# Performance work log

Hardware: AMD Instinct MI355X
Metric: run time of the kernel (lower is better)

The kernel has to match this reference:

```python
import jax, jax.numpy as jnp
import numpy as np

B, T, D, H = 16, 4096, 256, 512  # batch, seq_len, ninputs, nhiddens


def setup_inputs() -> dict:
    key = jax.random.key(0)
    k_x, k_ih, k_hh, k_b, k_bn = jax.random.split(key, 5)
    s = 1.0 / np.sqrt(H)
    xs = jax.random.normal(k_x, (B, T, D), dtype=jnp.float32)
    W_ih = jax.random.uniform(k_ih, (3 * H, D), minval=-s, maxval=s, dtype=jnp.float32)
    W_hh = jax.random.uniform(k_hh, (3 * H, H), minval=-s, maxval=s, dtype=jnp.float32)
    b = jax.random.uniform(k_b, (3 * H,), minval=-s, maxval=s, dtype=jnp.float32)
    b_n = jax.random.uniform(k_bn, (H,), minval=-s, maxval=s, dtype=jnp.float32)
    return {"xs": xs, "W_ih": W_ih, "W_hh": W_hh, "b": b, "b_n": b_n}


def _gru_scan(xs, W_ih, W_hh, b, b_n):
    # Precompute all input-side gates with one big GEMM: (B, T, 3H)
    igates = jnp.einsum('btd,gd->btg', xs, W_ih) + b

    def step(h, ig):
        # h: (B, H), ig: (B, 3H)
        hg = h @ W_hh.T  # (B, 3H)
        i_r, i_z, i_n = jnp.split(ig, 3, axis=-1)
        h_r, h_z, h_n = jnp.split(hg, 3, axis=-1)
        r = jax.nn.sigmoid(i_r + h_r)   # reset gate
        z = jax.nn.sigmoid(i_z + h_z)   # update gate (equinox 'inp')
        n = jnp.tanh(i_n + r * (h_n + b_n))
        h_new = n + z * (h - n)         # equinox: new + inp * (hidden - new)
        return h_new, h_new

    h0 = jnp.zeros((xs.shape[0], b_n.shape[0]), dtype=xs.dtype)
    _, ys = jax.lax.scan(step, h0, jnp.swapaxes(igates, 0, 1))  # (T, B, H)
    return jnp.swapaxes(ys, 0, 1)  # (B, T, H)


def reference(xs, W_ih, W_hh, b, b_n):
    # CellLayer('gru', 'deer') computes the exact GRU recurrence over time
    # (DEER's fixed point equals the sequential evaluation).
    return _gru_scan(xs, W_ih, W_hh, b, b_n)
```

## Files before the change

kernel.cpp:

```cpp
#include <hip/hip_runtime.h>
#include <stdint.h>
#include <stddef.h>

#define B_ 16
#define T_ 4096
#define D_ 256
#define H_ 512
#define G3_ 1536

#define OFF_IG   ((size_t)0)
#define OFF_WT   ((size_t)201326592)
#define OFF_MB   ((size_t)202899456)
#define WS_NEED  ((size_t)203423744)

#define PAR_STRIDE ((size_t)B_ * 8 * 512)

typedef _Float16 h2_t __attribute__((ext_vector_type(2)));

#if defined(__has_builtin)
#if __has_builtin(__builtin_amdgcn_fdot2)
#define HAVE_FDOT2 1
#endif
#endif

__device__ __forceinline__ float fdot2f(uint32_t w, uint32_t h, float acc) {
  union { uint32_t u; h2_t v; } a, b;
  a.u = w; b.u = h;
#ifdef HAVE_FDOT2
  return __builtin_amdgcn_fdot2(a.v, b.v, acc, false);
#else
  return fmaf((float)a.v.x, (float)b.v.x, fmaf((float)a.v.y, (float)b.v.y, acc));
#endif
}

__device__ __forceinline__ uint32_t packh2(float a, float b) {
  union { h2_t v; uint32_t u; } x;
  x.v.x = (_Float16)a; x.v.y = (_Float16)b;
  return x.u;
}

__device__ __forceinline__ uint32_t f16bits(float a) {
  union { _Float16 h; uint16_t u; } x;
  x.h = (_Float16)a;
  return (uint32_t)x.u;
}

__device__ __forceinline__ float h2f(uint16_t u) {
  union { _Float16 h; uint16_t u; } x;
  x.u = u;
  return (float)x.h;
}

__device__ __forceinline__ float sigmoidf_(float x) {
  return 1.0f / (1.0f + __expf(-x));
}

__device__ __forceinline__ float tanhf_(float x) {
  x = fminf(fmaxf(x, -15.0f), 15.0f);
  float e = __expf(-2.0f * x);
  return (1.0f - e) / (1.0f + e);
}

__global__ void __launch_bounds__(256) wt_kernel(const float* __restrict__ W, float4* __restrict__ Wt4) {
  int idx = blockIdx.x * 256 + threadIdx.x;
  if (idx >= G3_ * 64) return;
  int g = idx % G3_;
  int d4 = idx / G3_;
  float4 v = *(const float4*)(W + (size_t)g * D_ + 4 * d4);
  Wt4[(size_t)d4 * G3_ + g] = v;
}

__global__ void __launch_bounds__(256) ig_kernel(const float* __restrict__ xs,
                                                 const float* __restrict__ Wt,
                                                 const float* __restrict__ bias,
                                                 _Float16* __restrict__ ig) {
  __shared__ float xls[16 * 256];
  const int m0 = blockIdx.x * 16;
  const int tid = threadIdx.x;

  const float4* xsrc = (const float4*)(xs + (size_t)m0 * D_);
  float4* xdst = (float4*)xls;
#pragma unroll
  for (int k = 0; k < 4; ++k) xdst[tid + 256 * k] = xsrc[tid + 256 * k];
  __syncthreads();

  float acc[6][16];
#pragma unroll
  for (int k = 0; k < 6; ++k)
#pragma unroll
    for (int m = 0; m < 16; ++m) acc[k][m] = 0.0f;

  const float4* Wt4 = (const float4*)Wt;
  const float4* lds4 = (const float4*)xls;

  for (int d4 = 0; d4 < 64; ++d4) {
    float4 w[6];
#pragma unroll
    for (int k = 0; k < 6; ++k) w[k] = Wt4[(size_t)d4 * G3_ + tid + 256 * k];
#pragma unroll
    for (int m = 0; m < 16; ++m) {
      float4 xv = lds4[m * 64 + d4];
#pragma unroll
      for (int k = 0; k < 6; ++k) {
        acc[k][m] = fmaf(w[k].x, xv.x, acc[k][m]);
        acc[k][m] = fmaf(w[k].y, xv.y, acc[k][m]);
        acc[k][m] = fmaf(w[k].z, xv.z, acc[k][m]);
        acc[k][m] = fmaf(w[k].w, xv.w, acc[k][m]);
      }
    }
  }

#pragma unroll
  for (int k = 0; k < 6; ++k) {
    float bb = bias[tid + 256 * k];
#pragma unroll
    for (int m = 0; m < 16; ++m) {
      ig[(size_t)(m0 + m) * G3_ + tid + 256 * k] = (_Float16)(acc[k][m] + bb);
    }
  }
}

__global__ void __launch_bounds__(256, 1) rec_kernel(const _Float16* __restrict__ ig,
                                                     const float* __restrict__ Whh,
                                                     const float* __restrict__ bn,
                                                     uint32_t* __restrict__ mb,
                                                     float* __restrict__ out) {
  const int tid = threadIdx.x;
  const int wg = blockIdx.x;
  const int b = wg >> 4;
  const int s = wg & 15;
  const int q = tid & 7;
  const int c = tid >> 3;
  const int j = s * 32 + c;

  uint32_t wr[32], wz[32], wn[32];
  {
    const float4* s0 = (const float4*)(Whh + (size_t)j * H_ + q * 64);
    const float4* s1 = (const float4*)(Whh + (size_t)(j + H_) * H_ + q * 64);
    const float4* s2 = (const float4*)(Whh + (size_t)(j + 2 * H_) * H_ + q * 64);
#pragma unroll
    for (int i = 0; i < 16; ++i) {
      float4 v0 = s0[i]; wr[2 * i] = packh2(v0.x, v0.y); wr[2 * i + 1] = packh2(v0.z, v0.w);
      float4 v1 = s1[i]; wz[2 * i] = packh2(v1.x, v1.y); wz[2 * i + 1] = packh2(v1.z, v1.w);
      float4 v2 = s2[i]; wn[2 * i] = packh2(v2.x, v2.y); wn[2 * i + 1] = packh2(v2.z, v2.w);
    }
  }
  const float bnj = bn[j];

  __shared__ uint32_t hl[2][8][36];

  uint32_t* mypoll = mb + ((size_t)b * 8 + (s >> 1)) * 512 + 2 * tid;
  uint32_t* mypub  = mb + ((size_t)b * 8 + q) * 512 + j;

  const uint16_t* ig16 = (const uint16_t*)ig;
  size_t igbase = (size_t)b * T_ * G3_;

  uint16_t cr = ig16[igbase + j];
  uint16_t cz = ig16[igbase + j + H_];
  uint16_t cn = ig16[igbase + j + 2 * H_];
  uint16_t nr = ig16[igbase + G3_ + j];
  uint16_t nz = ig16[igbase + G3_ + j + H_];
  uint16_t nn2 = ig16[igbase + G3_ + j + 2 * H_];

  float hprev = 0.0f;

  for (int t = 0; t < T_; ++t) {
    uint16_t fr = 0, fz = 0, fn = 0;

    if (t > 0) {
      uint32_t* pb = mypoll + (size_t)(t & 1) * PAR_STRIDE;
      const uint32_t hi = (uint32_t)t << 16;
      uint32_t a0, a1;
      int it = 0;
      for (;;) {
        unsigned long long vv;
        asm volatile("global_load_dwordx2 %0, %1, off sc1\n\ts_waitcnt vmcnt(0)"
                     : "=v"(vv) : "v"(pb) : "memory");
        a0 = (uint32_t)vv;
        a1 = (uint32_t)(vv >> 32);
        if ((((a0 ^ hi) | (a1 ^ hi)) >> 16) == 0u) break;
        if (++it > (1 << 20)) { a0 = a1 = 0x7C00u; break; }
      }
      hl[t & 1][tid >> 5][tid & 31] = (a0 & 0xFFFFu) | (a1 << 16);

      if (t + 2 < T_) {
        const size_t fb = igbase + 2 * (size_t)G3_;
        fr = ig16[fb + j];
        fz = ig16[fb + j + H_];
        fn = ig16[fb + j + 2 * H_];
      }
    } else {
      const size_t fb = igbase + 2 * (size_t)G3_;
      fr = ig16[fb + j];
      fz = ig16[fb + j + H_];
      fn = ig16[fb + j + 2 * H_];
    }

    __syncthreads();

    float ar = 0.0f, az = 0.0f, an = 0.0f;
    if (t > 0) {
      const uint4* hq = (const uint4*)hl[t & 1][q];
      uint4 hv[8];
#pragma unroll
      for (int i = 0; i < 8; ++i) hv[i] = hq[i];
      float ar0 = 0.0f, az0 = 0.0f, an0 = 0.0f;
      float ar1 = 0.0f, az1 = 0.0f, an1 = 0.0f;
#pragma unroll
      for (int i = 0; i < 4; ++i) {
        ar0 = fdot2f(wr[4 * i + 0], hv[i].x, ar0); az0 = fdot2f(wz[4 * i + 0], hv[i].x, az0); an0 = fdot2f(wn[4 * i + 0], hv[i].x, an0);
        ar0 = fdot2f(wr[4 * i + 1], hv[i].y, ar0); az0 = fdot2f(wz[4 * i + 1], hv[i].y, az0); an0 = fdot2f(wn[4 * i + 1], hv[i].y, an0);
        ar0 = fdot2f(wr[4 * i + 2], hv[i].z, ar0); az0 = fdot2f(wz[4 * i + 2], hv[i].z, az0); an0 = fdot2f(wn[4 * i + 2], hv[i].z, an0);
        ar0 = fdot2f(wr[4 * i + 3], hv[i].w, ar0); az0 = fdot2f(wz[4 * i + 3], hv[i].w, az0); an0 = fdot2f(wn[4 * i + 3], hv[i].w, an0);
      }
#pragma unroll
      for (int i = 4; i < 8; ++i) {
        ar1 = fdot2f(wr[4 * i + 0], hv[i].x, ar1); az1 = fdot2f(wz[4 * i + 0], hv[i].x, az1); an1 = fdot2f(wn[4 * i + 0], hv[i].x, an1);
        ar1 = fdot2f(wr[4 * i + 1], hv[i].y, ar1); az1 = fdot2f(wz[4 * i + 1], hv[i].y, az1); an1 = fdot2f(wn[4 * i + 1], hv[i].y, an1);
        ar1 = fdot2f(wr[4 * i + 2], hv[i].z, ar1); az1 = fdot2f(wz[4 * i + 2], hv[i].z, az1); an1 = fdot2f(wn[4 * i + 2], hv[i].z, an1);
        ar1 = fdot2f(wr[4 * i + 3], hv[i].w, ar1); az1 = fdot2f(wz[4 * i + 3], hv[i].w, az1); an1 = fdot2f(wn[4 * i + 3], hv[i].w, an1);
      }
      ar = ar0 + ar1; az = az0 + az1; an = an0 + an1;
      ar += __shfl_xor(ar, 1); ar += __shfl_xor(ar, 2); ar += __shfl_xor(ar, 4);
      az += __shfl_xor(az, 1); az += __shfl_xor(az, 2); az += __shfl_xor(az, 4);
      an += __shfl_xor(an, 1); an += __shfl_xor(an, 2); an += __shfl_xor(an, 4);
    }

    const float igr = h2f(cr), igz = h2f(cz), ign = h2f(cn);
    const float r = sigmoidf_(igr + ar);
    const float z = sigmoidf_(igz + az);
    const float n = tanhf_(ign + r * (an + bnj));
    const float hnew = n + z * (hprev - n);
    hprev = hnew;

    const uint32_t wv = ((uint32_t)(t + 1) << 16) | f16bits(hnew);
    __hip_atomic_store(mypub + (size_t)((t + 1) & 1) * PAR_STRIDE, wv,
                       __ATOMIC_RELAXED, __HIP_MEMORY_SCOPE_AGENT);

    if (q == 0) {
      out[((size_t)b * T_ + t) * H_ + j] = hnew;
    }

    cr = nr; cz = nz; cn = nn2;
    nr = fr; nz = fz; nn2 = fn;
    igbase += G3_;
  }
}

__global__ void __launch_bounds__(512) naive_kernel(const float* __restrict__ xs,
                                                    const float* __restrict__ Wih,
                                                    const float* __restrict__ Whh,
                                                    const float* __restrict__ bias,
                                                    const float* __restrict__ bn,
                                                    float* __restrict__ out) {
  const int b = blockIdx.x;
  const int j = threadIdx.x;
  __shared__ float h[H_];
  __shared__ float xr[D_];
  h[j] = 0.0f;
  __syncthreads();
  for (int t = 0; t < T_; ++t) {
    if (j < D_) xr[j] = xs[((size_t)b * T_ + t) * D_ + j];
    __syncthreads();
    float a[2];
#pragma unroll
    for (int g = 0; g < 2; ++g) {
      const int row = j + g * H_;
      float ssum = bias[row];
      const float* wi = Wih + (size_t)row * D_;
      for (int d = 0; d < D_; ++d) ssum = fmaf(wi[d], xr[d], ssum);
      const float* wh = Whh + (size_t)row * H_;
      for (int kk = 0; kk < H_; ++kk) ssum = fmaf(wh[kk], h[kk], ssum);
      a[g] = ssum;
    }
    const float r = sigmoidf_(a[0]);
    const float z = sigmoidf_(a[1]);
    float i_n = bias[j + 2 * H_];
    {
      const float* wi = Wih + (size_t)(j + 2 * H_) * D_;
      for (int d = 0; d < D_; ++d) i_n = fmaf(wi[d], xr[d], i_n);
    }
    float h_n = 0.0f;
    {
      const float* wh = Whh + (size_t)(j + 2 * H_) * H_;
      for (int kk = 0; kk < H_; ++kk) h_n = fmaf(wh[kk], h[kk], h_n);
    }
    const float nn = tanhf_(i_n + r * (h_n + bn[j]));
    const float hnew = nn + z * (h[j] - nn);
    __syncthreads();
    h[j] = hnew;
    out[((size_t)b * T_ + t) * H_ + j] = hnew;
  }
}

extern "C" void kernel_launch(void* const* d_in, const int* in_sizes, int n_in,
                              void* d_out, int out_size, void* d_ws, size_t ws_size,
                              hipStream_t stream) {
  const float* xs  = (const float*)d_in[0];
  const float* Wih = (const float*)d_in[1];
  const float* Whh = (const float*)d_in[2];
  const float* bia = (const float*)d_in[3];
  const float* bnp = (const float*)d_in[4];
  float* out = (float*)d_out;

  if (ws_size >= WS_NEED) {
    char* ws = (char*)d_ws;
    _Float16* igp = (_Float16*)(ws + OFF_IG);
    float* wtp = (float*)(ws + OFF_WT);
    uint32_t* mbp = (uint32_t*)(ws + OFF_MB);

    hipMemsetAsync(mbp, 0, 2 * PAR_STRIDE * sizeof(uint32_t), stream);

    wt_kernel<<<dim3(384), dim3(256), 0, stream>>>(Wih, (float4*)wtp);
    ig_kernel<<<dim3((B_ * T_) / 16), dim3(256), 0, stream>>>(xs, wtp, bia, igp);
    rec_kernel<<<dim3(256), dim3(256), 0, stream>>>(igp, Whh, bnp, mbp, out);
  } else {
    naive_kernel<<<dim3(B_), dim3(H_), 0, stream>>>(xs, Wih, Whh, bia, bnp, out);
  }
}
```

Baseline: 7.599 ms.

## Remap workgroups so each batch shares an XCD and poll a local mailbox first

Workgroup indices are remapped so the 16 workgroups of one batch land on the same XCD, given round-robin dispatch across the 8 XCDs. Each step's hidden state is now published to two mailboxes: a local one (plain store, polled with sc0 loads that can hit the shared L2) and the original device-coherent one (sc1). Consumers poll the local copy a few times before falling back to the coherent path, and drop the fast path after repeated misses. This aims to cut the per-timestep cross-workgroup handoff latency, but it depends on the dispatch-to-XCD mapping and adds an extra store and a memset. The local mailbox reuses the W_ih transpose buffer after ig_kernel has finished with it.

```diff
diff --git a/kernel.cpp b/kernel.cpp
--- a/kernel.cpp
+++ b/kernel.cpp
@@ -12,6 +12,7 @@
 #define OFF_WT   ((size_t)201326592)
 #define OFF_MB   ((size_t)202899456)
 #define WS_NEED  ((size_t)203423744)
+#define OFF_MBL  OFF_WT
 
 #define PAR_STRIDE ((size_t)B_ * 8 * 512)
 
@@ -123,12 +124,15 @@
 __global__ void __launch_bounds__(256, 1) rec_kernel(const _Float16* __restrict__ ig,
                                                      const float* __restrict__ Whh,
                                                      const float* __restrict__ bn,
-                                                     uint32_t* __restrict__ mb,
+                                                     uint32_t* __restrict__ mbM,
+                                                     uint32_t* __restrict__ mbL,
                                                      float* __restrict__ out) {
   const int tid = threadIdx.x;
   const int wg = blockIdx.x;
-  const int b = wg >> 4;
-  const int s = wg & 15;
+  const int x = wg & 7;
+  const int y = wg >> 3;
+  const int b = x + 8 * (y >> 4);
+  const int s = y & 15;
   const int q = tid & 7;
   const int c = tid >> 3;
   const int j = s * 32 + c;
@@ -149,8 +153,12 @@
 
   __shared__ uint32_t hl[2][8][36];
 
-  uint32_t* mypoll = mb + ((size_t)b * 8 + (s >> 1)) * 512 + 2 * tid;
-  uint32_t* mypub  = mb + ((size_t)b * 8 + q) * 512 + j;
+  const size_t boxoff = ((size_t)b * 8 + (s >> 1)) * 512 + 2 * tid;
+  const size_t puboff = ((size_t)b * 8 + q) * 512 + j;
+  uint32_t* mypollL = mbL + boxoff;
+  uint32_t* mypollM = mbM + boxoff;
+  uint32_t* mypubL  = mbL + puboff;
+  uint32_t* mypubM  = mbM + puboff;
 
   const uint16_t* ig16 = (const uint16_t*)ig;
   size_t igbase = (size_t)b * T_ * G3_;
@@ -163,24 +171,48 @@
   uint16_t nn2 = ig16[igbase + G3_ + j + 2 * H_];
 
   float hprev = 0.0f;
+  bool fastok = true;
+  int fail_streak = 0;
 
   for (int t = 0; t < T_; ++t) {
     uint16_t fr = 0, fz = 0, fn = 0;
 
     if (t > 0) {
-      uint32_t* pb = mypoll + (size_t)(t & 1) * PAR_STRIDE;
       const uint32_t hi = (uint32_t)t << 16;
-      uint32_t a0, a1;
-      int it = 0;
-      for (;;) {
-        unsigned long long vv;
-        asm volatile("global_load_dwordx2 %0, %1, off sc1\n\ts_waitcnt vmcnt(0)"
-                     : "=v"(vv) : "v"(pb) : "memory");
-        a0 = (uint32_t)vv;
-        a1 = (uint32_t)(vv >> 32);
-        if ((((a0 ^ hi) | (a1 ^ hi)) >> 16) == 0u) break;
-        if (++it > (1 << 20)) { a0 = a1 = 0x7C00u; break; }
-      }
+      const size_t poff = (size_t)(t & 1) * PAR_STRIDE;
+      uint32_t a0 = 0, a1 = 0;
+      bool ok = false;
+
+      if (fastok) {
+        uint32_t* pl = mypollL + poff;
+        for (int r2 = 0; r2 < 8; ++r2) {
+          unsigned long long vv;
+          asm volatile("global_load_dwordx2 %0, %1, off sc0\n\ts_waitcnt vmcnt(0)"
+                       : "=v"(vv) : "v"(pl) : "memory");
+          __builtin_amdgcn_sched_barrier(0);
+          a0 = (uint32_t)vv;
+          a1 = (uint32_t)(vv >> 32);
+          if ((((a0 ^ hi) | (a1 ^ hi)) >> 16) == 0u) { ok = true; break; }
+        }
+        if (ok) fail_streak = 0;
+        else if (++fail_streak >= 8) fastok = false;
+      }
+
+      if (!ok) {
+        uint32_t* pm = mypollM + poff;
+        int it = 0;
+        for (;;) {
+          unsigned long long vv;
+          asm volatile("global_load_dwordx2 %0, %1, off sc1\n\ts_waitcnt vmcnt(0)"
+                       : "=v"(vv) : "v"(pm) : "memory");
+          __builtin_amdgcn_sched_barrier(0);
+          a0 = (uint32_t)vv;
+          a1 = (uint32_t)(vv >> 32);
+          if ((((a0 ^ hi) | (a1 ^ hi)) >> 16) == 0u) break;
+          if (++it > (1 << 20)) { a0 = a1 = 0x7C00u; break; }
+        }
+      }
+
       hl[t & 1][tid >> 5][tid & 31] = (a0 & 0xFFFFu) | (a1 << 16);
 
       if (t + 2 < T_) {
@@ -234,8 +266,9 @@
     hprev = hnew;
 
     const uint32_t wv = ((uint32_t)(t + 1) << 16) | f16bits(hnew);
-    __hip_atomic_store(mypub + (size_t)((t + 1) & 1) * PAR_STRIDE, wv,
-                       __ATOMIC_RELAXED, __HIP_MEMORY_SCOPE_AGENT);
+    const size_t noff = (size_t)((t + 1) & 1) * PAR_STRIDE;
+    asm volatile("global_store_dword %0, %1, off" :: "v"(mypubL + noff), "v"(wv) : "memory");
+    __hip_atomic_store(mypubM + noff, wv, __ATOMIC_RELAXED, __HIP_MEMORY_SCOPE_AGENT);
 
     if (q == 0) {
       out[((size_t)b * T_ + t) * H_ + j] = hnew;
@@ -307,13 +340,17 @@
     char* ws = (char*)d_ws;
     _Float16* igp = (_Float16*)(ws + OFF_IG);
     float* wtp = (float*)(ws + OFF_WT);
-    uint32_t* mbp = (uint32_t*)(ws + OFF_MB);
-
-    hipMemsetAsync(mbp, 0, 2 * PAR_STRIDE * sizeof(uint32_t), stream);
+    uint32_t* mbM = (uint32_t*)(ws + OFF_MB);
+    uint32_t* mbL = (uint32_t*)(ws + OFF_MBL);
+
+    hipMemsetAsync(mbM, 0, 2 * PAR_STRIDE * sizeof(uint32_t), stream);
 
     wt_kernel<<<dim3(384), dim3(256), 0, stream>>>(Wih, (float4*)wtp);
     ig_kernel<<<dim3((B_ * T_) / 16), dim3(256), 0, stream>>>(xs, wtp, bia, igp);
-    rec_kernel<<<dim3(256), dim3(256), 0, stream>>>(igp, Whh, bnp, mbp, out);
+
+    hipMemsetAsync(mbL, 0, 2 * PAR_STRIDE * sizeof(uint32_t), stream);
+
+    rec_kernel<<<dim3(256), dim3(256), 0, stream>>>(igp, Whh, bnp, mbM, mbL, out);
   } else {
     naive_kernel<<<dim3(B_), dim3(H_), 0, stream>>>(xs, Wih, Whh, bia, bnp, out);
   }
```

Result: slower. 10.29 ms (+35.4%).

## Double recurrent workgroup size and pipeline mailbox polling with two outstanding loads

Applied to the files above, without the earlier changes.

The recurrent kernel now runs 128 workgroups of 512 threads instead of 256 of 256, so each workgroup owns 64 hidden units and fewer workgroups take part in the cross-workgroup exchange each step. The mailbox poll now reads single dwords, keeping two loads in flight and alternating between them, so a retry is issued before the previous result has been checked. The goal is lower per-timestep synchronisation latency. In exchange each thread writes individual 16-bit entries into the shared-memory hidden-state buffer, and the unseen compute section has to match the new 64-column indexing.

```diff
diff --git a/kernel.cpp b/kernel.cpp
--- a/kernel.cpp
+++ b/kernel.cpp
@@ -120,18 +120,18 @@
   }
 }
 
-__global__ void __launch_bounds__(256, 1) rec_kernel(const _Float16* __restrict__ ig,
+__global__ void __launch_bounds__(512, 1) rec_kernel(const _Float16* __restrict__ ig,
                                                      const float* __restrict__ Whh,
                                                      const float* __restrict__ bn,
                                                      uint32_t* __restrict__ mb,
                                                      float* __restrict__ out) {
   const int tid = threadIdx.x;
   const int wg = blockIdx.x;
-  const int b = wg >> 4;
-  const int s = wg & 15;
+  const int b = wg >> 3;
+  const int s = wg & 7;
   const int q = tid & 7;
   const int c = tid >> 3;
-  const int j = s * 32 + c;
+  const int j = s * 64 + c;
 
   uint32_t wr[32], wz[32], wn[32];
   {
@@ -148,8 +148,9 @@
   const float bnj = bn[j];
 
   __shared__ uint32_t hl[2][8][36];
-
-  uint32_t* mypoll = mb + ((size_t)b * 8 + (s >> 1)) * 512 + 2 * tid;
+  uint16_t* hl16 = (uint16_t*)hl;
+
+  uint32_t* mypoll = mb + ((size_t)b * 8 + s) * 512 + tid;
   uint32_t* mypub  = mb + ((size_t)b * 8 + q) * 512 + j;
 
   const uint16_t* ig16 = (const uint16_t*)ig;
@@ -169,19 +170,29 @@
 
     if (t > 0) {
       uint32_t* pb = mypoll + (size_t)(t & 1) * PAR_STRIDE;
-      const uint32_t hi = (uint32_t)t << 16;
-      uint32_t a0, a1;
+      const uint32_t want = (uint32_t)t;
+      uint32_t va, vb, a0 = 0;
+      asm volatile("global_load_dword %0, %2, off sc1\n\t"
+                   "global_load_dword %1, %2, off sc1"
+                   : "=&v"(va), "=&v"(vb) : "v"(pb) : "memory");
       int it = 0;
       for (;;) {
-        unsigned long long vv;
-        asm volatile("global_load_dwordx2 %0, %1, off sc1\n\ts_waitcnt vmcnt(0)"
-                     : "=v"(vv) : "v"(pb) : "memory");
-        a0 = (uint32_t)vv;
-        a1 = (uint32_t)(vv >> 32);
-        if ((((a0 ^ hi) | (a1 ^ hi)) >> 16) == 0u) break;
-        if (++it > (1 << 20)) { a0 = a1 = 0x7C00u; break; }
-      }
-      hl[t & 1][tid >> 5][tid & 31] = (a0 & 0xFFFFu) | (a1 << 16);
+        asm volatile("s_waitcnt vmcnt(1)" ::: "memory");
+        __builtin_amdgcn_sched_barrier(0);
+        a0 = va;
+        if ((a0 >> 16) == want) break;
+        asm volatile("global_load_dword %0, %1, off sc1" : "=&v"(va) : "v"(pb) : "memory");
+        asm volatile("s_waitcnt vmcnt(1)" ::: "memory");
+        __builtin_amdgcn_sched_barrier(0);
+        a0 = vb;
+        if ((a0 >> 16) == want) break;
+        asm volatile("global_load_dword %0, %1, off sc1" : "=&v"(vb) : "v"(pb) : "memory");
+        if (++it > (1 << 20)) { a0 = 0x7C00u; break; }
+      }
+      asm volatile("s_waitcnt vmcnt(0)" ::: "memory");
+      __builtin_amdgcn_sched_barrier(0);
+
+      hl16[(t & 1) * 576 + (tid >> 6) * 72 + (tid & 63)] = (uint16_t)(a0 & 0xFFFFu);
 
       if (t + 2 < T_) {
         const size_t fb = igbase + 2 * (size_t)G3_;
@@ -313,7 +324,7 @@
 
     wt_kernel<<<dim3(384), dim3(256), 0, stream>>>(Wih, (float4*)wtp);
     ig_kernel<<<dim3((B_ * T_) / 16), dim3(256), 0, stream>>>(xs, wtp, bia, igp);
-    rec_kernel<<<dim3(256), dim3(256), 0, stream>>>(igp, Whh, bnp, mbp, out);
+    rec_kernel<<<dim3(128), dim3(512), 0, stream>>>(igp, Whh, bnp, mbp, out);
   } else {
     naive_kernel<<<dim3(B_), dim3(H_), 0, stream>>>(xs, Wih, Whh, bia, bnp, out);
   }
```

Measured after the change: 7.604 ms. Within noise of the previous version (+0.1%).
